# Optimization experiments

Measured on AMD Instinct MI355X. Metric: run time of the kernel, lower is better.

Reference implementation:

```python
import jax, jax.numpy as jnp
import numpy as np
from jax import lax

CONF_THR = 0.5
NMS_THR = 0.5
B, N, C = 2, 8192, 80


def setup_inputs() -> dict:
    key = jax.random.key(0)
    k1, k2, k3, k4 = jax.random.split(key, 4)
    cls_logits = jax.random.normal(k1, (B, N, C), dtype=jnp.float32)
    deltas = jax.random.normal(k2, (B, N, 4), dtype=jnp.float32) * 0.1
    # anchors: valid x1,y1,x2,y2 boxes in [0,1]
    ctr = jax.random.uniform(k3, (N, 2), minval=0.05, maxval=0.95)
    wh = jax.random.uniform(k4, (N, 2), minval=0.02, maxval=0.2)
    anchors = jnp.concatenate([ctr - 0.5 * wh, ctr + 0.5 * wh], axis=-1).astype(jnp.float32)
    return {"cls_logits": cls_logits, "deltas": deltas, "anchors": anchors}


def apply_deltas_to_anchors(deltas, anchors):
    aw = anchors[:, 2] - anchors[:, 0]
    ah = anchors[:, 3] - anchors[:, 1]
    acx = anchors[:, 0] + 0.5 * aw
    acy = anchors[:, 1] + 0.5 * ah
    dx, dy = deltas[..., 0], deltas[..., 1]
    dw = jnp.minimum(deltas[..., 2], 4.0)
    dh = jnp.minimum(deltas[..., 3], 4.0)
    pcx = dx * aw + acx
    pcy = dy * ah + acy
    pw = jnp.exp(dw) * aw
    ph = jnp.exp(dh) * ah
    boxes = jnp.stack([pcx - 0.5 * pw, pcy - 0.5 * ph,
                       pcx + 0.5 * pw, pcy + 0.5 * ph], axis=-1)
    return jnp.clip(boxes, 0.0, 1.0)


def iou_matrix(b):  # b: [N,4] -> [N,N]
    x1, y1, x2, y2 = b[:, 0], b[:, 1], b[:, 2], b[:, 3]
    area = (x2 - x1) * (y2 - y1)
    ix1 = jnp.maximum(x1[:, None], x1[None, :])
    iy1 = jnp.maximum(y1[:, None], y1[None, :])
    ix2 = jnp.minimum(x2[:, None], x2[None, :])
    iy2 = jnp.minimum(y2[:, None], y2[None, :])
    inter = jnp.clip(ix2 - ix1, 0.0) * jnp.clip(iy2 - iy1, 0.0)
    union = area[:, None] + area[None, :] - inter
    return inter / jnp.maximum(union, 1e-9)


def nms_keep(boxes, scores, valid, thr):
    """Greedy NMS; returns bool keep mask in original order (padded shape N)."""
    n = boxes.shape[0]
    order = jnp.argsort(-scores)
    bs = boxes[order]
    vs = valid[order]
    iou = iou_matrix(bs)  # [N,N] in score order
    idx = jnp.arange(n)

    def body(keep, i):
        suppressed = jnp.any((iou[i] > thr) & keep & (idx < i))
        k = vs[i] & ~suppressed
        keep = keep.at[i].set(k)
        return keep, None

    keep_sorted, _ = lax.scan(body, jnp.zeros(n, dtype=bool), idx)
    return jnp.zeros(n, dtype=bool).at[order].set(keep_sorted)


def reference(cls_logits, deltas, anchors):
    all_scores = jax.nn.sigmoid(cls_logits)                 # [B,N,C]
    boxes = apply_deltas_to_anchors(deltas, anchors)        # [B,N,4]
    max_scores = jnp.max(all_scores, axis=-1)               # [B,N]
    labels = jnp.argmax(all_scores, axis=-1)                # [B,N]
    conf_mask = max_scores > CONF_THR
    w = boxes[..., 2] - boxes[..., 0]
    h = boxes[..., 3] - boxes[..., 1]
    size_mask = (w > 0.01) & (h > 0.01) & (w < 0.99) & (h < 0.99)
    valid = conf_mask & size_mask
    keep = jax.vmap(nms_keep, in_axes=(0, 0, 0, None))(boxes, max_scores, valid, NMS_THR)
    # Padded (jit-friendly) equivalent of the ragged per-image outputs:
    return boxes, max_scores, labels, keep, all_scores
```

## Files before the change

kernel.cpp:

```cpp
#include <hip/hip_runtime.h>

constexpr int NB = 2;
constexpr int NN = 8192;
constexpr int NC = 80;
constexpr int ROWS = NN + 1;

constexpr size_t OFF_BOXES  = 0;
constexpr size_t OFF_SCORES = (size_t)NB * NN * 4;
constexpr size_t OFF_LABELS = OFF_SCORES + (size_t)NB * NN;
constexpr size_t OFF_KEEP   = OFF_LABELS + (size_t)NB * NN;
constexpr size_t OFF_ALL    = OFF_KEEP + (size_t)NB * NN;

constexpr size_t WS_KEYS  = 0;
constexpr size_t WS_VBYTE = WS_KEYS + (size_t)NB * NN * 8;
constexpr size_t WS_ORDER = WS_VBYTE + (size_t)NB * NN;
constexpr size_t WS_SBOX  = WS_ORDER + (size_t)NB * NN * 4;
constexpr size_t WS_VBITS = WS_SBOX + (size_t)NB * NN * 16;
constexpr size_t WS_MASK  = WS_VBITS + (size_t)NB * 128 * 8;
constexpr size_t WS_DNM   = WS_MASK + (size_t)NB * ROWS * 128 * 8;
constexpr size_t WS_PART  = WS_DNM + (size_t)NB * 128 * 4 * 64 * 8;
constexpr size_t WS_TOTAL = WS_PART + (size_t)NB * 8 * NN * 4;
constexpr size_t WS_TOTAL_OLD = WS_PART;
constexpr int DNM_WORDS = NB * 128 * 4 * 64;
constexpr int NSEG = 8;

typedef unsigned long long u64;
typedef __attribute__((ext_vector_type(2))) unsigned long long u64x2;

__device__ inline void lbar() {
  __builtin_amdgcn_s_waitcnt(0xc07f);
  __builtin_amdgcn_s_barrier();
}

__device__ inline u64 readlane64(u64 v, int src) {
  unsigned int lo = (unsigned int)__builtin_amdgcn_readlane((int)(unsigned int)v, src);
  unsigned int hi = (unsigned int)__builtin_amdgcn_readlane((int)(unsigned int)(v >> 32), src);
  return ((u64)hi << 32) | lo;
}

__device__ inline u64 readfirstlane64(u64 v) {
  unsigned int lo = (unsigned int)__builtin_amdgcn_readfirstlane((int)(unsigned int)v);
  unsigned int hi = (unsigned int)__builtin_amdgcn_readfirstlane((int)(unsigned int)(v >> 32));
  return ((u64)hi << 32) | lo;
}

__device__ inline float iou_pair(const float4 p, const float4 q) {
#pragma clang fp contract(off)
  float areaA = (p.z - p.x) * (p.w - p.y);
  float areaB = (q.z - q.x) * (q.w - q.y);
  float ix1 = fmaxf(p.x, q.x);
  float iy1 = fmaxf(p.y, q.y);
  float ix2 = fminf(p.z, q.z);
  float iy2 = fminf(p.w, q.w);
  float inter = fmaxf(ix2 - ix1, 0.0f) * fmaxf(iy2 - iy1, 0.0f);
  float uni = areaA + areaB - inter;
  return inter / fmaxf(uni, 1e-9f);
}

__device__ inline float clip01(float v) { return fminf(fmaxf(v, 0.0f), 1.0f); }

__global__ __launch_bounds__(256) void decode_kernel(
    const float* __restrict__ logits, const float4* __restrict__ deltas,
    const float4* __restrict__ anchors, float4* __restrict__ boxes_out,
    float* __restrict__ scores_out, float* __restrict__ labels_out,
    float* __restrict__ all_out, u64* __restrict__ keys,
    unsigned char* __restrict__ vbyte, u64* __restrict__ vbits) {
#pragma clang fp contract(off)
  if (blockIdx.x == 0 && threadIdx.x < NB * 128) vbits[threadIdx.x] = 0ull;
  int wid = (blockIdx.x * 256 + threadIdx.x) >> 6;
  int lane = threadIdx.x & 63;
  int n = wid & (NN - 1);
  size_t base = (size_t)wid * NC;

  float x0 = logits[base + lane];
  float sig0 = 1.0f / (1.0f + expf(-x0));
  all_out[base + lane] = sig0;
  float bs = sig0;
  int bidx = lane;
  if (lane < NC - 64) {
    float x1 = logits[base + 64 + lane];
    float sig1 = 1.0f / (1.0f + expf(-x1));
    all_out[base + 64 + lane] = sig1;
    if (sig1 > bs) { bs = sig1; bidx = lane + 64; }
  }
  for (int off = 32; off; off >>= 1) {
    float os = __shfl_xor(bs, off, 64);
    int oi = __shfl_xor(bidx, off, 64);
    if (os > bs || (os == bs && oi < bidx)) { bs = os; bidx = oi; }
  }
  if (lane == 0) {
    float4 d = deltas[wid];
    float4 a = anchors[n];
    float aw = a.z - a.x, ah = a.w - a.y;
    float acx = a.x + 0.5f * aw, acy = a.y + 0.5f * ah;
    float dw = fminf(d.z, 4.0f), dh = fminf(d.w, 4.0f);
    float pcx = d.x * aw + acx;
    float pcy = d.y * ah + acy;
    float pw = expf(dw) * aw;
    float ph = expf(dh) * ah;
    float4 bx;
    bx.x = clip01(pcx - 0.5f * pw);
    bx.y = clip01(pcy - 0.5f * ph);
    bx.z = clip01(pcx + 0.5f * pw);
    bx.w = clip01(pcy + 0.5f * ph);
    boxes_out[wid] = bx;
    scores_out[wid] = bs;
    labels_out[wid] = (float)bidx;
    float bw = bx.z - bx.x, bh = bx.w - bx.y;
    bool valid = (bs > 0.5f) && (bw > 0.01f) && (bh > 0.01f) &&
                 (bw < 0.99f) && (bh < 0.99f);
    vbyte[wid] = valid ? 1 : 0;
    keys[wid] = ((u64)__float_as_uint(bs) << 32) | (unsigned int)(NN - 1 - n);
  }
}

__global__ __launch_bounds__(1024) void rank_part_kernel(
    const u64* __restrict__ keys, int* __restrict__ part,
    u64* __restrict__ dnm) {
  int b = blockIdx.z, seg = blockIdx.y, rb = blockIdx.x;
  int gid = ((blockIdx.z * NSEG + blockIdx.y) * gridDim.x + blockIdx.x) * 1024 +
            threadIdx.x;
  if (gid < DNM_WORDS) dnm[gid] = 0ull;
  int r = threadIdx.x & 255;
  int q = threadIdx.x >> 8;
  int i = rb * 256 + r;
  const u64* kb = keys + (size_t)b * NN;
  u64 myk = kb[i];
  int cnt = 0;
  int j0 = seg * (NN / NSEG) + q * (NN / NSEG / 4);
  int j1 = j0 + NN / NSEG / 4;
#pragma unroll 8
  for (int j = j0; j < j1; ++j) {
    u64 kj = kb[j];
    cnt += (kj > myk) ? 1 : 0;
  }
  __shared__ unsigned short partl[4][256];
  partl[q][r] = (unsigned short)cnt;
  __syncthreads();
  if (threadIdx.x < 256) {
    int s = partl[0][r] + partl[1][r] + partl[2][r] + partl[3][r];
    part[((size_t)b * NSEG + seg) * NN + i] = s;
  }
}

__global__ __launch_bounds__(256) void rank_final_kernel(
    const int* __restrict__ part, const float4* __restrict__ boxes,
    const unsigned char* __restrict__ vbyte, int* __restrict__ order,
    float4* __restrict__ sbox, u64* __restrict__ vbits) {
  int b = blockIdx.y;
  int i = blockIdx.x * 256 + threadIdx.x;
  const int* pb = part + (size_t)b * NSEG * NN + i;
  int rank = 0;
#pragma unroll
  for (int s = 0; s < NSEG; ++s) rank += pb[(size_t)s * NN];
  order[(size_t)b * NN + rank] = i;
  sbox[(size_t)b * NN + rank] = boxes[(size_t)b * NN + i];
  if (vbyte[(size_t)b * NN + i])
    atomicOr(&vbits[b * 128 + (rank >> 6)], 1ull << (rank & 63));
}

__global__ __launch_bounds__(1024) void rank_kernel(
    const u64* __restrict__ keys, const float4* __restrict__ boxes,
    const unsigned char* __restrict__ vbyte, int* __restrict__ order,
    float4* __restrict__ sbox, u64* __restrict__ vbits,
    u64* __restrict__ dnm) {
  int b = blockIdx.y;
  int gid = (blockIdx.y * gridDim.x + blockIdx.x) * 1024 + threadIdx.x;
  for (int z = gid; z < DNM_WORDS; z += 65536) dnm[z] = 0ull;
  int r = threadIdx.x & 255;
  int q = threadIdx.x >> 8;
  int i = blockIdx.x * 256 + r;
  const u64* kb = keys + (size_t)b * NN;
  u64 myk = kb[i];
  int cnt = 0;
  int j0 = q * (NN / 4), j1 = j0 + NN / 4;
#pragma unroll 8
  for (int j = j0; j < j1; ++j) {
    u64 kj = kb[j];
    cnt += (kj > myk) ? 1 : 0;
  }
  __shared__ unsigned short part[4][256];
  part[q][r] = (unsigned short)cnt;
  __syncthreads();
  if (threadIdx.x < 256) {
    int rank = part[0][r] + part[1][r] + part[2][r] + part[3][r];
    order[(size_t)b * NN + rank] = i;
    sbox[(size_t)b * NN + rank] = boxes[(size_t)b * NN + i];
    if (vbyte[(size_t)b * NN + i])
      atomicOr(&vbits[b * 128 + (rank >> 6)], 1ull << (rank & 63));
  }
}

__global__ __launch_bounds__(64) void build_kernel(
    const float4* __restrict__ sbox, u64* __restrict__ mask,
    u64* __restrict__ dnm) {
  int byq = blockIdx.y, bxq = blockIdx.x, b = blockIdx.z;
  int by, bx;
  if (bxq >= byq) {
    by = byq; bx = bxq;
  } else if (byq == 64) {
    return;
  } else {
    by = 128 - byq; bx = 127 - bxq;
  }
  int lane = threadIdx.x;
  __shared__ float4 cb[64];
  cb[lane] = sbox[(size_t)b * NN + bx * 64 + lane];
  __syncthreads();
  int i = by * 64 + lane;
  float4 rb = sbox[(size_t)b * NN + i];
  u64 word = 0;
  if (bx == by) {
    for (int jj = 0; jj < 64; ++jj)
      if (iou_pair(rb, cb[jj]) > 0.5f) word |= 1ull << jj;
    word &= ~(1ull << lane);
    u64 lmask = (1ull << lane) - 1ull;
    mask[((size_t)b * ROWS + i) * 128 + bx] = word & ~lmask;
    dnm[(((size_t)b * 128 + by) * 4 + 0) * 64 + lane] = word & lmask;
  } else {
    for (int jj = 0; jj < 64; ++jj)
      if (iou_pair(rb, cb[jj]) > 0.5f) word |= 1ull << jj;
    mask[((size_t)b * ROWS + i) * 128 + bx] = word;
    int dq = bx - by;
    if (dq < 4) dnm[(((size_t)b * 128 + by) * 4 + dq) * 64 + lane] = word;
  }
}

struct TSet {
  u64x2 t0, t1, t2, t3, t4, t5, t6, t7, t8, t9;
};

__global__ __launch_bounds__(512) void reduce_kernel(
    u64* __restrict__ mask, const u64* __restrict__ vbits,
    const u64* __restrict__ dnm, const int* __restrict__ order,
    float* __restrict__ keep_out) {
  int b = blockIdx.x, tid = threadIdx.x;
  int lane = tid & 63, wave = tid >> 6;
  __shared__ u64 s_remv[128];
  __shared__ u64 s_keep[128];
  __shared__ int s_rowlist[2][80];
  u64* mbz = mask + (size_t)b * ROWS * 128;
  const u64* mb = mbz;
  const u64* dn = dnm + (size_t)b * 128 * 4 * 64;

  for (int w = tid; w < 128; w += 512) {
    s_remv[w] = 0ull;
    mbz[(size_t)NN * 128 + w] = 0ull;
  }
  if (tid < 160) s_rowlist[tid / 80][tid % 80] = NN;

  u64 va = 0, vb2 = 0;
  u64 dA = 0, nA = 0, mA = 0, oA = 0, dB = 0, nB = 0, mB = 0, oB = 0;
  u64 dC = 0, nC = 0, mC = 0, oC = 0, dD = 0, nD = 0, mD = 0, oD = 0;
  if (wave == 0) {
    va = vbits[b * 128 + 2 * lane];
    vb2 = vbits[b * 128 + 2 * lane + 1];
    const u64* r0 = dn + lane;
    dA = r0[0]; nA = r0[64]; mA = r0[128]; oA = r0[192];
    const u64* r1 = dn + 4 * 64 + lane;
    dB = r1[0]; nB = r1[64]; mB = r1[128]; oB = r1[192];
  }
  TSet U{}, V{};
  int w0i = 2 * lane;
  __syncthreads();

  auto serial_body = [&](int c, u64 dcur, u64 ncur, u64 mcur, u64 ocur,
                         u64& dnew, u64& nnew, u64& mnew, u64& onew) {
    int cp = (c + 2 < 128) ? (c + 2) : 127;
    u64 pa = (u64)(uintptr_t)(dn + (size_t)cp * 4 * 64 + lane);
    asm volatile(
        "global_load_dwordx2 %0, %4, off\n\t"
        "global_load_dwordx2 %1, %4, off offset:512\n\t"
        "global_load_dwordx2 %2, %4, off offset:1024\n\t"
        "global_load_dwordx2 %3, %4, off offset:1536"
        : "=&v"(dnew), "=&v"(nnew), "=&v"(mnew), "=&v"(onew)
        : "v"(pa)
        : "memory");
    int par = c & 1;
    u64 rm = s_remv[c];
    u64 vbw = readlane64(par ? vb2 : va, c >> 1);
    u64 cand = readfirstlane64(vbw & ~rm);
    asm volatile("s_waitcnt vmcnt(8)"
                 : "+v"(dcur), "+v"(ncur), "+v"(mcur), "+v"(ocur)
                 :
                 : "memory");
    __builtin_amdgcn_sched_barrier(0);
    u64 kept = cand;
    while (true) {
      u64 sup = __ballot((dcur & kept) != 0ull);
      u64 nk = cand & ~sup;
      if (nk == kept) break;
      kept = nk;
    }
    bool isk = (kept >> lane) & 1;
    if (c + 1 < 128 && isk && ncur) atomicOr(&s_remv[c + 1], ncur);
    if (c + 2 < 128 && isk && mcur) atomicOr(&s_remv[c + 2], mcur);
    if (c + 3 < 128 && isk && ocur) atomicOr(&s_remv[c + 3], ocur);
    s_rowlist[par][lane] = NN;
    if (isk) {
      int pos = __popcll(kept & ((1ull << lane) - 1ull));
      s_rowlist[par][pos] = c * 64 + lane;
    }
    if (lane == 0) s_keep[c] = kept;
  };

  auto bg_body = [&](int c, TSet& T) {
    asm volatile("s_waitcnt vmcnt(10)"
                 : "+v"(T.t0), "+v"(T.t1), "+v"(T.t2), "+v"(T.t3), "+v"(T.t4),
                   "+v"(T.t5), "+v"(T.t6), "+v"(T.t7), "+v"(T.t8), "+v"(T.t9)
                 :
                 : "memory");
    __builtin_amdgcn_sched_barrier(0);
    u64 ax = T.t0[0] | T.t1[0] | T.t2[0] | T.t3[0] | T.t4[0] | T.t5[0] |
             T.t6[0] | T.t7[0] | T.t8[0] | T.t9[0];
    u64 ay = T.t0[1] | T.t1[1] | T.t2[1] | T.t3[1] | T.t4[1] | T.t5[1] |
             T.t6[1] | T.t7[1] | T.t8[1] | T.t9[1];
    int sc = (c + 1) & ~1;
    int wx = sc + w0i, wy = wx + 1;
    if (wx > c && wx < 128 && ax) atomicOr(&s_remv[wx], ax);
    if (wy > c && wy < 128 && ay) atomicOr(&s_remv[wy], ay);
    const int* rl = s_rowlist[(c - 1) & 1];
    int base = wave - 1;
    int si = (c + 3) & ~1;
    int w = si + w0i;
    bool wok = w < 128;
    const u64* mw = mb + w;
    u64 zaddr = (u64)(uintptr_t)(mbz + (size_t)NN * 128);
    int r0 = rl[base], r1 = rl[base + 7], r2 = rl[base + 14],
        r3 = rl[base + 21], r4 = rl[base + 28], r5 = rl[base + 35],
        r6 = rl[base + 42], r7 = rl[base + 49], r8 = rl[base + 56],
        r9 = rl[base + 63];
    u64 a0 = (wok && r0 != NN) ? (u64)(uintptr_t)(mw + (size_t)r0 * 128) : zaddr;
    u64 a1 = (wok && r1 != NN) ? (u64)(uintptr_t)(mw + (size_t)r1 * 128) : zaddr;
    u64 a2 = (wok && r2 != NN) ? (u64)(uintptr_t)(mw + (size_t)r2 * 128) : zaddr;
    u64 a3 = (wok && r3 != NN) ? (u64)(uintptr_t)(mw + (size_t)r3 * 128) : zaddr;
    u64 a4 = (wok && r4 != NN) ? (u64)(uintptr_t)(mw + (size_t)r4 * 128) : zaddr;
    u64 a5 = (wok && r5 != NN) ? (u64)(uintptr_t)(mw + (size_t)r5 * 128) : zaddr;
    u64 a6 = (wok && r6 != NN) ? (u64)(uintptr_t)(mw + (size_t)r6 * 128) : zaddr;
    u64 a7 = (wok && r7 != NN) ? (u64)(uintptr_t)(mw + (size_t)r7 * 128) : zaddr;
    u64 a8 = (wok && r8 != NN) ? (u64)(uintptr_t)(mw + (size_t)r8 * 128) : zaddr;
    u64 a9 = (wok && r9 != NN) ? (u64)(uintptr_t)(mw + (size_t)r9 * 128) : zaddr;
    asm volatile(
        "global_load_dwordx4 %0, %10, off\n\t"
        "global_load_dwordx4 %1, %11, off\n\t"
        "global_load_dwordx4 %2, %12, off\n\t"
        "global_load_dwordx4 %3, %13, off\n\t"
        "global_load_dwordx4 %4, %14, off\n\t"
        "global_load_dwordx4 %5, %15, off\n\t"
        "global_load_dwordx4 %6, %16, off\n\t"
        "global_load_dwordx4 %7, %17, off\n\t"
        "global_load_dwordx4 %8, %18, off\n\t"
        "global_load_dwordx4 %9, %19, off"
        : "=&v"(T.t0), "=&v"(T.t1), "=&v"(T.t2), "=&v"(T.t3), "=&v"(T.t4),
          "=&v"(T.t5), "=&v"(T.t6), "=&v"(T.t7), "=&v"(T.t8), "=&v"(T.t9)
        : "v"(a0), "v"(a1), "v"(a2), "v"(a3), "v"(a4), "v"(a5), "v"(a6),
          "v"(a7), "v"(a8), "v"(a9)
        : "memory");
  };

  for (int c = 0; c < 128; c += 4) {
    if (wave == 0) serial_body(c, dA, nA, mA, oA, dC, nC, mC, oC);
    else bg_body(c, U);
    lbar();
    if (wave == 0) serial_body(c + 1, dB, nB, mB, oB, dD, nD, mD, oD);
    else bg_body(c + 1, V);
    lbar();
    if (wave == 0) serial_body(c + 2, dC, nC, mC, oC, dA, nA, mA, oA);
    else bg_body(c + 2, U);
    lbar();
    if (wave == 0) serial_body(c + 3, dD, nD, mD, oD, dB, nB, mB, oB);
    else bg_body(c + 3, V);
    lbar();
  }

  asm volatile("s_waitcnt vmcnt(0)" ::: "memory");

  for (int p = tid; p < NN; p += 512) {
    int orig = order[(size_t)b * NN + p];
    keep_out[(size_t)b * NN + orig] =
        ((s_keep[p >> 6] >> (p & 63)) & 1) ? 1.0f : 0.0f;
  }
}

__global__ __launch_bounds__(1024) void nms_fallback(
    const float4* __restrict__ sbox, const u64* __restrict__ vbits,
    const int* __restrict__ order, float* __restrict__ keep_out) {
  int b = blockIdx.x, tid = threadIdx.x;
  __shared__ u64 dead[128];
  __shared__ int s_next;
  __shared__ float4 s_box;
  for (int w = tid; w < 128; w += 1024) dead[w] = ~vbits[b * 128 + w];
  for (int p = tid; p < NN; p += 1024)
    keep_out[(size_t)b * NN + order[(size_t)b * NN + p]] = 0.0f;
  __syncthreads();
  int i = 0;
  while (true) {
    if (tid == 0) {
      int nxt = NN;
      int w = i >> 6;
      u64 live = ~dead[w] & (~0ull << (i & 63));
      while (true) {
        if (live) { nxt = w * 64 + __builtin_ctzll(live); break; }
        if (++w >= 128) break;
        live = ~dead[w];
      }
      s_next = nxt;
      if (nxt < NN) {
        s_box = sbox[(size_t)b * NN + nxt];
        keep_out[(size_t)b * NN + order[(size_t)b * NN + nxt]] = 1.0f;
      }
    }
    __syncthreads();
    i = s_next;
    if (i >= NN) break;
    float4 kb = s_box;
    for (int j = i + 1 + tid; j < NN; j += 1024) {
      if (iou_pair(kb, sbox[(size_t)b * NN + j]) > 0.5f)
        atomicOr(&dead[j >> 6], 1ull << (j & 63));
    }
    __syncthreads();
    i = i + 1;
  }
}

extern "C" void kernel_launch(void* const* d_in, const int* in_sizes, int n_in,
                              void* d_out, int out_size, void* d_ws, size_t ws_size,
                              hipStream_t stream) {
  const float* logits = (const float*)d_in[0];
  const float4* deltas = (const float4*)d_in[1];
  const float4* anchors = (const float4*)d_in[2];
  float* out = (float*)d_out;
  float4* boxes_out = (float4*)(out + OFF_BOXES);
  float* scores_out = out + OFF_SCORES;
  float* labels_out = out + OFF_LABELS;
  float* keep_out = out + OFF_KEEP;
  float* all_out = out + OFF_ALL;

  char* ws = (char*)d_ws;
  u64* keys = (u64*)(ws + WS_KEYS);
  unsigned char* vbyte = (unsigned char*)(ws + WS_VBYTE);
  int* order = (int*)(ws + WS_ORDER);
  float4* sbox = (float4*)(ws + WS_SBOX);
  u64* vbits = (u64*)(ws + WS_VBITS);
  u64* mask = (u64*)(ws + WS_MASK);
  u64* dnm = (u64*)(ws + WS_DNM);
  int* part = (int*)(ws + WS_PART);

  decode_kernel<<<dim3(NB * NN / 4), dim3(256), 0, stream>>>(
      logits, deltas, anchors, boxes_out, scores_out, labels_out, all_out,
      keys, vbyte, vbits);
  if (ws_size >= WS_TOTAL) {
    rank_part_kernel<<<dim3(NN / 256, NSEG, NB), dim3(1024), 0, stream>>>(
        keys, part, dnm);
    rank_final_kernel<<<dim3(NN / 256, NB), dim3(256), 0, stream>>>(
        part, (const float4*)boxes_out, vbyte, order, sbox, vbits);
    build_kernel<<<dim3(128, 65, NB), dim3(64), 0, stream>>>(sbox, mask, dnm);
    reduce_kernel<<<dim3(NB), dim3(512), 0, stream>>>(mask, vbits, dnm, order,
                                                      keep_out);
  } else if (ws_size >= WS_TOTAL_OLD) {
    rank_kernel<<<dim3(NN / 256, NB), dim3(1024), 0, stream>>>(
        keys, (const float4*)boxes_out, vbyte, order, sbox, vbits, dnm);
    build_kernel<<<dim3(128, 65, NB), dim3(64), 0, stream>>>(sbox, mask, dnm);
    reduce_kernel<<<dim3(NB), dim3(512), 0, stream>>>(mask, vbits, dnm, order,
                                                      keep_out);
  } else {
    rank_kernel<<<dim3(NN / 256, NB), dim3(1024), 0, stream>>>(
        keys, (const float4*)boxes_out, vbyte, order, sbox, vbits, dnm);
    nms_fallback<<<dim3(NB), dim3(1024), 0, stream>>>(sbox, vbits, order,
                                                      keep_out);
  }
}
```

Baseline: 264.5 us.

## Add sparse CSR suppression lists for NMS reduce with dense fallback on overflow

Adds a fill_csr kernel that compresses each row of the upper-triangular IoU bitmask into a list of 16-bit column indices using a wave prefix sum and a global atomic allocator. A new single-wave reduce_sparse kernel walks the chunks serially, resolving in-chunk suppression with ballots. For each kept box it ORs that box's sparse suppression list into the shared removal mask, so it no longer streams full mask rows. The dense reducer now runs only when the CSR buffer overflows, and the keep scatter moves to a separate kernel. The cost is two extra launches, a CSR build pass over the whole mask, and a larger workspace requirement, which falls back to the old path if the workspace is too small.

Result: slower. 382.2 us (+44.5%).

```diff
diff --git a/kernel.cpp b/kernel.cpp
--- a/kernel.cpp
+++ b/kernel.cpp
@@ -21,6 +21,11 @@
 constexpr size_t WS_PART  = WS_DNM + (size_t)NB * 128 * 4 * 64 * 8;
 constexpr size_t WS_TOTAL = WS_PART + (size_t)NB * 8 * NN * 4;
 constexpr size_t WS_TOTAL_OLD = WS_PART;
+constexpr unsigned CSR_CAP = 1u << 20;
+constexpr size_t WS_RD  = WS_TOTAL;
+constexpr size_t WS_CSR = WS_RD + (size_t)NB * NN * 8;
+constexpr size_t WS_CNT = WS_CSR + (size_t)NB * (CSR_CAP + 16) * 2;
+constexpr size_t WS_TOTAL_SPARSE = WS_CNT + 64;
 constexpr int DNM_WORDS = NB * 128 * 4 * 64;
 constexpr int NSEG = 8;
 
@@ -116,26 +121,27 @@
 
 __global__ __launch_bounds__(1024) void rank_part_kernel(
     const u64* __restrict__ keys, int* __restrict__ part,
-    u64* __restrict__ dnm) {
+    u64* __restrict__ dnm, unsigned int* cnt, unsigned int* ovf) {
   int b = blockIdx.z, seg = blockIdx.y, rb = blockIdx.x;
   int gid = ((blockIdx.z * NSEG + blockIdx.y) * gridDim.x + blockIdx.x) * 1024 +
             threadIdx.x;
   if (gid < DNM_WORDS) dnm[gid] = 0ull;
+  if (cnt && gid < NB) { cnt[gid] = 0u; ovf[gid] = 0u; }
   int r = threadIdx.x & 255;
   int q = threadIdx.x >> 8;
   int i = rb * 256 + r;
   const u64* kb = keys + (size_t)b * NN;
   u64 myk = kb[i];
-  int cnt = 0;
+  int cnt2 = 0;
   int j0 = seg * (NN / NSEG) + q * (NN / NSEG / 4);
   int j1 = j0 + NN / NSEG / 4;
 #pragma unroll 8
   for (int j = j0; j < j1; ++j) {
     u64 kj = kb[j];
-    cnt += (kj > myk) ? 1 : 0;
+    cnt2 += (kj > myk) ? 1 : 0;
   }
   __shared__ unsigned short partl[4][256];
-  partl[q][r] = (unsigned short)cnt;
+  partl[q][r] = (unsigned short)cnt2;
   __syncthreads();
   if (threadIdx.x < 256) {
     int s = partl[0][r] + partl[1][r] + partl[2][r] + partl[3][r];
@@ -226,15 +232,171 @@
   }
 }
 
+__global__ __launch_bounds__(1024) void fill_csr(
+    const u64* __restrict__ mask, u64* __restrict__ rd,
+    unsigned short* __restrict__ csr, unsigned int* __restrict__ cnt,
+    unsigned int* __restrict__ ovf) {
+  int lane = threadIdx.x & 63;
+  int gw = blockIdx.x * 16 + (threadIdx.x >> 6);
+  int b = gw >> 13;
+  int r = gw & (NN - 1);
+  const u64* row = mask + ((size_t)b * ROWS + r) * 128;
+  int cd = r >> 6;
+  int w0 = 2 * lane;
+  u64x2 v = *(const u64x2*)(row + w0);
+  u64 x0 = (w0 >= cd) ? v[0] : 0ull;
+  u64 x1 = (w0 + 1 >= cd) ? v[1] : 0ull;
+  int c2 = __popcll(x0) + __popcll(x1);
+  int pre = c2;
+  for (int off = 1; off < 64; off <<= 1) {
+    int t = __shfl_up(pre, off, 64);
+    if (lane >= off) pre += t;
+  }
+  int excl = pre - c2;
+  int tot = __shfl(pre, 63, 64);
+  unsigned atot = ((unsigned)tot + 7u) & ~7u;
+  unsigned base = 0;
+  if (lane == 0 && tot > 0) base = atomicAdd(&cnt[b], atot);
+  base = (unsigned)__shfl((int)base, 0, 64);
+  bool ok = (base + atot <= CSR_CAP);
+  if (lane == 0) {
+    if (tot > 0 && !ok) atomicOr(&ovf[b], 1u);
+    rd[(size_t)b * NN + r] = ok ? ((u64)base | ((u64)(unsigned)tot << 32)) : 0ull;
+  }
+  if (ok && tot > 0) {
+    unsigned short* dst = csr + (size_t)b * (CSR_CAP + 16) + base + excl;
+    int k = 0;
+    u64 t0 = x0;
+    while (t0) {
+      int bit = __builtin_ctzll(t0);
+      dst[k++] = (unsigned short)(w0 * 64 + bit);
+      t0 &= t0 - 1;
+    }
+    u64 t1 = x1;
+    while (t1) {
+      int bit = __builtin_ctzll(t1);
+      dst[k++] = (unsigned short)((w0 + 1) * 64 + bit);
+      t1 &= t1 - 1;
+    }
+  }
+}
+
+__global__ __launch_bounds__(64) void reduce_sparse(
+    const u64* __restrict__ vbits, const u64* __restrict__ dnm,
+    const u64* __restrict__ rdarr, const unsigned short* __restrict__ csr,
+    const unsigned int* __restrict__ ovf, u64* __restrict__ keepw) {
+  int b = blockIdx.x, lane = threadIdx.x;
+  if (ovf[b]) return;
+  __shared__ u64 s_remv[128];
+  __shared__ u64 s_keep[128];
+  s_remv[2 * lane] = 0ull;
+  s_remv[2 * lane + 1] = 0ull;
+  u64 va = vbits[b * 128 + 2 * lane];
+  u64 vb2 = vbits[b * 128 + 2 * lane + 1];
+  const u64* dnb = dnm + (size_t)b * 128 * 4 * 64;
+  const u64* rdb = rdarr + (size_t)b * NN;
+  const unsigned short* cb = csr + (size_t)b * (CSR_CAP + 16);
+
+  u64 rdv0 = rdb[lane];
+  u64 rdv1 = rdb[64 + lane];
+  u64 rdS2 = rdb[128 + lane];
+  u64 rdS3 = rdb[192 + lane];
+  unsigned offS0 = (unsigned)rdv0; int degS0 = (int)(rdv0 >> 32);
+  unsigned offS1 = (unsigned)rdv1; int degS1 = (int)(rdv1 >> 32);
+  u64 dS0 = dnb[lane];
+  u64 dS1 = dnb[4 * 64 + lane];
+  u64x2 eaS0 = *(const u64x2*)(cb + offS0);
+  u64x2 ebS0 = *(const u64x2*)(cb + offS0 + 8);
+  u64x2 eaS1 = *(const u64x2*)(cb + offS1);
+  u64x2 ebS1 = *(const u64x2*)(cb + offS1 + 8);
+  u64 rdS0 = 0, rdS1 = 0, dS2 = 0, dS3 = 0;
+  u64x2 eaS2{}, ebS2{}, eaS3{}, ebS3{};
+  unsigned offS2 = 0, offS3 = 0;
+  int degS2 = 0, degS3 = 0;
+  __syncthreads();
+  asm volatile("s_waitcnt vmcnt(0)" ::: "memory");
+  __builtin_amdgcn_sched_barrier(0);
+
+  auto body = [&](int c, u64x2 ea, u64x2 eb, u64 dcur, unsigned offCur,
+                  int degCur, u64 rdNext, u64& rdOut, u64x2& eaOut,
+                  u64x2& ebOut, u64& dOut, unsigned& offOut, int& degOut) {
+    asm volatile("s_waitcnt vmcnt(4)"
+                 : "+v"(ea), "+v"(eb), "+v"(dcur), "+v"(rdNext)
+                 :
+                 : "memory");
+    __builtin_amdgcn_sched_barrier(0);
+    offOut = (unsigned)rdNext;
+    degOut = (int)(rdNext >> 32);
+    int cp2 = (c + 2 < 128) ? c + 2 : 127;
+    int cp4 = (c + 4 < 128) ? c + 4 : 127;
+    u64 a_rd = (u64)(uintptr_t)(rdb + (size_t)cp4 * 64 + lane);
+    u64 a_e = (u64)(uintptr_t)(cb + offOut);
+    u64 a_d = (u64)(uintptr_t)(dnb + ((size_t)cp2 * 4) * 64 + lane);
+    asm volatile(
+        "global_load_dwordx2 %0, %4, off\n\t"
+        "global_load_dwordx4 %1, %5, off\n\t"
+        "global_load_dwordx4 %2, %5, off offset:16\n\t"
+        "global_load_dwordx2 %3, %6, off"
+        : "=&v"(rdOut), "=&v"(eaOut), "=&v"(ebOut), "=&v"(dOut)
+        : "v"(a_rd), "v"(a_e), "v"(a_d)
+        : "memory");
+    u64 rm = s_remv[c];
+    u64 vbw = readlane64((c & 1) ? vb2 : va, c >> 1);
+    u64 cand = readfirstlane64(vbw & ~rm);
+    u64 kept = cand;
+    while (true) {
+      u64 sup = __ballot((dcur & kept) != 0ull);
+      u64 nk = cand & ~sup;
+      if (nk == kept) break;
+      kept = nk;
+    }
+    bool isk = (kept >> lane) & 1;
+    if (isk && degCur > 0) {
+      int kmax = degCur < 16 ? degCur : 16;
+      u64 w0 = ea[0], w1 = ea[1], w2 = eb[0], w3 = eb[1];
+#pragma unroll
+      for (int k = 0; k < 16; ++k) {
+        if (k < kmax) {
+          u64 src = (k < 4) ? w0 : (k < 8) ? w1 : (k < 12) ? w2 : w3;
+          int j = (int)((src >> (16 * (k & 3))) & 0xFFFFull);
+          atomicOr(&s_remv[j >> 6], 1ull << (j & 63));
+        }
+      }
+      for (int k = 16; k < degCur; ++k) {
+        int j = cb[offCur + k];
+        atomicOr(&s_remv[j >> 6], 1ull << (j & 63));
+      }
+    }
+    if (lane == 0) s_keep[c] = kept;
+  };
+
+  for (int c = 0; c < 128; c += 4) {
+    body(c + 0, eaS0, ebS0, dS0, offS0, degS0, rdS2, rdS0, eaS2, ebS2, dS2,
+         offS2, degS2);
+    body(c + 1, eaS1, ebS1, dS1, offS1, degS1, rdS3, rdS1, eaS3, ebS3, dS3,
+         offS3, degS3);
+    body(c + 2, eaS2, ebS2, dS2, offS2, degS2, rdS0, rdS2, eaS0, ebS0, dS0,
+         offS0, degS0);
+    body(c + 3, eaS3, ebS3, dS3, offS3, degS3, rdS1, rdS3, eaS1, ebS1, dS1,
+         offS1, degS1);
+  }
+
+  asm volatile("s_waitcnt vmcnt(0)" ::: "memory");
+  __syncthreads();
+  keepw[b * 128 + 2 * lane] = s_keep[2 * lane];
+  keepw[b * 128 + 2 * lane + 1] = s_keep[2 * lane + 1];
+}
+
 struct TSet {
   u64x2 t0, t1, t2, t3, t4, t5, t6, t7, t8, t9;
 };
 
-__global__ __launch_bounds__(512) void reduce_kernel(
+__global__ __launch_bounds__(512) void reduce_dense(
     u64* __restrict__ mask, const u64* __restrict__ vbits,
-    const u64* __restrict__ dnm, const int* __restrict__ order,
-    float* __restrict__ keep_out) {
+    const u64* __restrict__ dnm, const unsigned int* __restrict__ ovf,
+    u64* __restrict__ keepw) {
   int b = blockIdx.x, tid = threadIdx.x;
+  if (ovf && ovf[b] == 0) return;
   int lane = tid & 63, wave = tid >> 6;
   __shared__ u64 s_remv[128];
   __shared__ u64 s_keep[128];
@@ -374,12 +536,18 @@
   }
 
   asm volatile("s_waitcnt vmcnt(0)" ::: "memory");
-
-  for (int p = tid; p < NN; p += 512) {
-    int orig = order[(size_t)b * NN + p];
-    keep_out[(size_t)b * NN + orig] =
-        ((s_keep[p >> 6] >> (p & 63)) & 1) ? 1.0f : 0.0f;
-  }
+  __syncthreads();
+  for (int w = tid; w < 128; w += 512) keepw[b * 128 + w] = s_keep[w];
+}
+
+__global__ __launch_bounds__(256) void scatter_keep(
+    const u64* __restrict__ keepw, const int* __restrict__ order,
+    float* __restrict__ keep_out) {
+  int b = blockIdx.y;
+  int p = blockIdx.x * 256 + threadIdx.x;
+  int orig = order[(size_t)b * NN + p];
+  keep_out[(size_t)b * NN + orig] =
+      ((keepw[b * 128 + (p >> 6)] >> (p & 63)) & 1) ? 1.0f : 0.0f;
 }
 
 __global__ __launch_bounds__(1024) void nms_fallback(
@@ -445,24 +613,47 @@
   u64* mask = (u64*)(ws + WS_MASK);
   u64* dnm = (u64*)(ws + WS_DNM);
   int* part = (int*)(ws + WS_PART);
+  u64* rdarr = (u64*)(ws + WS_RD);
+  unsigned short* csr = (unsigned short*)(ws + WS_CSR);
+  unsigned int* cnt = (unsigned int*)(ws + WS_CNT);
+  unsigned int* ovf = cnt + NB;
+  u64* keepw = (u64*)(ws + WS_KEYS);
 
   decode_kernel<<<dim3(NB * NN / 4), dim3(256), 0, stream>>>(
       logits, deltas, anchors, boxes_out, scores_out, labels_out, all_out,
       keys, vbyte, vbits);
-  if (ws_size >= WS_TOTAL) {
+  if (ws_size >= WS_TOTAL_SPARSE) {
     rank_part_kernel<<<dim3(NN / 256, NSEG, NB), dim3(1024), 0, stream>>>(
-        keys, part, dnm);
+        keys, part, dnm, cnt, ovf);
     rank_final_kernel<<<dim3(NN / 256, NB), dim3(256), 0, stream>>>(
         part, (const float4*)boxes_out, vbyte, order, sbox, vbits);
     build_kernel<<<dim3(128, 65, NB), dim3(64), 0, stream>>>(sbox, mask, dnm);
-    reduce_kernel<<<dim3(NB), dim3(512), 0, stream>>>(mask, vbits, dnm, order,
-                                                      keep_out);
+    fill_csr<<<dim3(NB * NN / 16), dim3(1024), 0, stream>>>(mask, rdarr, csr,
+                                                            cnt, ovf);
+    reduce_sparse<<<dim3(NB), dim3(64), 0, stream>>>(vbits, dnm, rdarr, csr,
+                                                     ovf, keepw);
+    reduce_dense<<<dim3(NB), dim3(512), 0, stream>>>(mask, vbits, dnm, ovf,
+                                                     keepw);
+    scatter_keep<<<dim3(NN / 256, NB), dim3(256), 0, stream>>>(keepw, order,
+                                                               keep_out);
+  } else if (ws_size >= WS_TOTAL) {
+    rank_part_kernel<<<dim3(NN / 256, NSEG, NB), dim3(1024), 0, stream>>>(
+        keys, part, dnm, nullptr, nullptr);
+    rank_final_kernel<<<dim3(NN / 256, NB), dim3(256), 0, stream>>>(
+        part, (const float4*)boxes_out, vbyte, order, sbox, vbits);
+    build_kernel<<<dim3(128, 65, NB), dim3(64), 0, stream>>>(sbox, mask, dnm);
+    reduce_dense<<<dim3(NB), dim3(512), 0, stream>>>(mask, vbits, dnm, nullptr,
+                                                     keepw);
+    scatter_keep<<<dim3(NN / 256, NB), dim3(256), 0, stream>>>(keepw, order,
+                                                               keep_out);
   } else if (ws_size >= WS_TOTAL_OLD) {
     rank_kernel<<<dim3(NN / 256, NB), dim3(1024), 0, stream>>>(
         keys, (const float4*)boxes_out, vbyte, order, sbox, vbits, dnm);
     build_kernel<<<dim3(128, 65, NB), dim3(64), 0, stream>>>(sbox, mask, dnm);
-    reduce_kernel<<<dim3(NB), dim3(512), 0, stream>>>(mask, vbits, dnm, order,
-                                                      keep_out);
+    reduce_dense<<<dim3(NB), dim3(512), 0, stream>>>(mask, vbits, dnm, nullptr,
+                                                     keepw);
+    scatter_keep<<<dim3(NN / 256, NB), dim3(256), 0, stream>>>(keepw, order,
+                                                               keep_out);
   } else {
     rank_kernel<<<dim3(NN / 256, NB), dim3(1024), 0, stream>>>(
         keys, (const float4*)boxes_out, vbyte, order, sbox, vbits, dnm);
```
